# Performance work log

Measured on AMD Instinct MI355X. Metric: run time of the kernel, lower is better.

## Reference

```python
import jax, jax.numpy as jnp
import numpy as np

H = 128  # rnn_size

def _run_lstm(x, Wih, Whh, bih, bhh):
    # x: [B, T, D]; Wih: [4H, D]; Whh: [4H, H]; biases: [4H]
    B = x.shape[0]
    xg = jnp.einsum('btd,gd->btg', x, Wih) + bih + bhh  # precompute input projection [B,T,4H]
    WhhT = Whh.T  # [H, 4H]
    def step(carry, xg_t):
        h, c = carry
        g = xg_t + h @ WhhT  # [B, 4H]
        i = jax.nn.sigmoid(g[:, :H])
        f = jax.nn.sigmoid(g[:, H:2 * H])
        gg = jnp.tanh(g[:, 2 * H:3 * H])
        o = jax.nn.sigmoid(g[:, 3 * H:])
        c = f * c + i * gg
        h = o * jnp.tanh(c)
        return (h, c), h
    init = (jnp.zeros((B, H), x.dtype), jnp.zeros((B, H), x.dtype))
    _, ys = jax.lax.scan(step, init, jnp.swapaxes(xg, 0, 1))  # [T, B, H]
    return jnp.swapaxes(ys, 0, 1)  # [B, T, H]

def _bilstm(x, layers):
    h = x
    for (fw, bw) in layers:
        yf = _run_lstm(h, *fw)
        yb = jnp.flip(_run_lstm(jnp.flip(h, axis=1), *bw), axis=1)
        h = jnp.concatenate([yf, yb], axis=-1)  # [B, T, 2H]
    return h

def setup_inputs() -> dict:
    key = jax.random.key(0)
    ks = iter(jax.random.split(key, 32))
    B, T, D = 64, 512, 64
    s = 0.08  # init scale ~ 1/sqrt(H) to avoid gate saturation
    inp = {'x': jax.random.normal(next(ks), (B, T, D), jnp.float32)}
    for name, shape in [
        ('Wih00', (4 * H, D)), ('Whh00', (4 * H, H)), ('bih00', (4 * H,)), ('bhh00', (4 * H,)),
        ('Wih01', (4 * H, D)), ('Whh01', (4 * H, H)), ('bih01', (4 * H,)), ('bhh01', (4 * H,)),
        ('Wih10', (4 * H, 2 * H)), ('Whh10', (4 * H, H)), ('bih10', (4 * H,)), ('bhh10', (4 * H,)),
        ('Wih11', (4 * H, 2 * H)), ('Whh11', (4 * H, H)), ('bih11', (4 * H,)), ('bhh11', (4 * H,)),
        ('W1', (256, 2 * H)), ('b1', (256,)), ('W2', (D, 256)), ('b2', (D,)),
    ]:
        inp[name] = jax.random.normal(next(ks), shape, jnp.float32) * s
    return inp

def reference(x, Wih00, Whh00, bih00, bhh00, Wih01, Whh01, bih01, bhh01,
              Wih10, Whh10, bih10, bhh10, Wih11, Whh11, bih11, bhh11,
              W1, b1, W2, b2):
    layers = [((Wih00, Whh00, bih00, bhh00), (Wih01, Whh01, bih01, bhh01)),
              ((Wih10, Whh10, bih10, bhh10), (Wih11, Whh11, bih11, bhh11))]
    out = _bilstm(x, layers)  # [B, T, 2H]
    h = jax.nn.relu(jnp.einsum('bth,oh->bto', out, W1) + b1)
    return jnp.tanh(jnp.einsum('bth,oh->bto', h, W2) + b2)  # [B, T, input_size]
```

## Files before the change

### kernel.cpp

```cpp
#include <hip/hip_runtime.h>
#include <hip/hip_bf16.h>
#include <hip/hip_fp16.h>

typedef _Float16 h2vec __attribute__((ext_vector_type(2)));
typedef _Float16 f16x8 __attribute__((ext_vector_type(8)));
typedef float f32x4 __attribute__((ext_vector_type(4)));

static __device__ __forceinline__ float fast_sigmoid(float x) {
  return __builtin_amdgcn_rcpf(1.f + __expf(-x));
}
static __device__ __forceinline__ float fast_tanh(float x) {
  return 1.f - 2.f * __builtin_amdgcn_rcpf(__expf(2.f * x) + 1.f);
}
static __device__ __forceinline__ float fdot2u(unsigned int a, unsigned int b, float c) {
#if __has_builtin(__builtin_amdgcn_fdot2)
  return __builtin_amdgcn_fdot2(__builtin_bit_cast(h2vec, a),
                                __builtin_bit_cast(h2vec, b), c, false);
#else
  h2vec av = __builtin_bit_cast(h2vec, a);
  h2vec bv = __builtin_bit_cast(h2vec, b);
  return c + (float)av[0] * (float)bv[0] + (float)av[1] * (float)bv[1];
#endif
}
template<int CTRL>
static __device__ __forceinline__ float dpp_add(float v) {
  int x = __builtin_bit_cast(int, v);
  int y = __builtin_amdgcn_update_dpp(0, x, CTRL, 0xF, 0xF, true);
  return v + __builtin_bit_cast(float, y);
}
template<int CTRL>
static __device__ __forceinline__ float dpp_mov(float v) {
  int x = __builtin_bit_cast(int, v);
  int y = __builtin_amdgcn_update_dpp(0, x, CTRL, 0xF, 0xF, true);
  return __builtin_bit_cast(float, y);
}

template<int MODE>
__global__ __launch_bounds__(256) void gemm_mfma(
    const float* __restrict__ A, const float* __restrict__ W,
    const float* __restrict__ b0, const float* __restrict__ b1,
    float* __restrict__ C, int M, int N, int K) {
  __shared__ __align__(16) unsigned char As[128 * 128];
  __shared__ __align__(16) unsigned char Bs[64 * 128];
  const int tid = threadIdx.x;
  const int wave = tid >> 6, l = tid & 63;
  const int wm = wave >> 1, wn = wave & 1;
  const int m0 = blockIdx.x * 128, n0 = blockIdx.y * 64;
  const int lrow = l & 15, lq = l >> 4;

  f32x4 acc[4][2] = {};
  const int arow = tid >> 1, akc = (tid & 1) * 32;
  const int brow = tid >> 2, bkc = (tid & 3) * 16;

  for (int k0 = 0; k0 < K; k0 += 64) {
    {
      const float* src = A + (size_t)(m0 + arow) * K + k0 + akc;
#pragma unroll
      for (int u = 0; u < 4; ++u) {
        float4 v0 = *reinterpret_cast<const float4*>(src + u * 8);
        float4 v1 = *reinterpret_cast<const float4*>(src + u * 8 + 4);
        f16x8 h;
        h[0] = (_Float16)v0.x; h[1] = (_Float16)v0.y;
        h[2] = (_Float16)v0.z; h[3] = (_Float16)v0.w;
        h[4] = (_Float16)v1.x; h[5] = (_Float16)v1.y;
        h[6] = (_Float16)v1.z; h[7] = (_Float16)v1.w;
        const int kbyte = (akc + u * 8) * 2;
        *reinterpret_cast<f16x8*>(&As[arow * 128 + (kbyte ^ ((arow & 7) << 4))]) = h;
      }
    }
    {
      const float* src = W + (size_t)(n0 + brow) * K + k0 + bkc;
#pragma unroll
      for (int u = 0; u < 2; ++u) {
        float4 v0 = *reinterpret_cast<const float4*>(src + u * 8);
        float4 v1 = *reinterpret_cast<const float4*>(src + u * 8 + 4);
        f16x8 h;
        h[0] = (_Float16)v0.x; h[1] = (_Float16)v0.y;
        h[2] = (_Float16)v0.z; h[3] = (_Float16)v0.w;
        h[4] = (_Float16)v1.x; h[5] = (_Float16)v1.y;
        h[6] = (_Float16)v1.z; h[7] = (_Float16)v1.w;
        const int kbyte = (bkc + u * 8) * 2;
        *reinterpret_cast<f16x8*>(&Bs[brow * 128 + (kbyte ^ ((brow & 7) << 4))]) = h;
      }
    }
    __syncthreads();
#pragma unroll
    for (int kk = 0; kk < 64; kk += 32) {
      const int kbyte = (kk + lq * 8) * 2;
      f16x8 af[4], bf[2];
#pragma unroll
      for (int mt = 0; mt < 4; ++mt) {
        const int row = wm * 64 + mt * 16 + lrow;
        af[mt] = *reinterpret_cast<const f16x8*>(&As[row * 128 + (kbyte ^ ((row & 7) << 4))]);
      }
#pragma unroll
      for (int nt = 0; nt < 2; ++nt) {
        const int row = wn * 32 + nt * 16 + lrow;
        bf[nt] = *reinterpret_cast<const f16x8*>(&Bs[row * 128 + (kbyte ^ ((row & 7) << 4))]);
      }
#pragma unroll
      for (int mt = 0; mt < 4; ++mt)
#pragma unroll
        for (int nt = 0; nt < 2; ++nt)
          acc[mt][nt] = __builtin_amdgcn_mfma_f32_16x16x32_f16(af[mt], bf[nt], acc[mt][nt], 0, 0, 0);
    }
    __syncthreads();
  }

#pragma unroll
  for (int nt = 0; nt < 2; ++nt) {
    const int n = n0 + wn * 32 + nt * 16 + lrow;
    float bias = (MODE == 0) ? (b0[n] + b1[n]) : b0[n];
#pragma unroll
    for (int mt = 0; mt < 4; ++mt) {
#pragma unroll
      for (int r = 0; r < 4; ++r) {
        const int m = m0 + wm * 64 + mt * 16 + lq * 4 + r;
        float val = acc[mt][nt][r] + bias;
        if (MODE == 1) val = fmaxf(val, 0.f);
        if (MODE == 2) val = fast_tanh(val);
        C[(size_t)m * N + n] = val;
      }
    }
  }
}

__global__ __launch_bounds__(256) void gemm_proj_h(
    const float* __restrict__ A,
    const float* __restrict__ W0, const float* __restrict__ W1,
    const float* __restrict__ bi0, const float* __restrict__ bh0,
    const float* __restrict__ bi1, const float* __restrict__ bh1,
    __half* __restrict__ C0, __half* __restrict__ C1, int M, int N, int K) {
  const float* __restrict__ W  = blockIdx.z ? W1 : W0;
  const float* __restrict__ b0 = blockIdx.z ? bi1 : bi0;
  const float* __restrict__ b1 = blockIdx.z ? bh1 : bh0;
  __half* __restrict__ C = blockIdx.z ? C1 : C0;

  __shared__ __align__(16) unsigned char As[128 * 128];
  __shared__ __align__(16) unsigned char Bs[64 * 128];
  const int tid = threadIdx.x;
  const int wave = tid >> 6, l = tid & 63;
  const int wm = wave >> 1, wn = wave & 1;
  const int m0 = blockIdx.x * 128, n0 = blockIdx.y * 64;
  const int lrow = l & 15, lq = l >> 4;

  f32x4 acc[4][2] = {};
  const int arow = tid >> 1, akc = (tid & 1) * 32;
  const int brow = tid >> 2, bkc = (tid & 3) * 16;

  for (int k0 = 0; k0 < K; k0 += 64) {
    {
      const float* src = A + (size_t)(m0 + arow) * K + k0 + akc;
#pragma unroll
      for (int u = 0; u < 4; ++u) {
        float4 v0 = *reinterpret_cast<const float4*>(src + u * 8);
        float4 v1 = *reinterpret_cast<const float4*>(src + u * 8 + 4);
        f16x8 h;
        h[0] = (_Float16)v0.x; h[1] = (_Float16)v0.y;
        h[2] = (_Float16)v0.z; h[3] = (_Float16)v0.w;
        h[4] = (_Float16)v1.x; h[5] = (_Float16)v1.y;
        h[6] = (_Float16)v1.z; h[7] = (_Float16)v1.w;
        const int kbyte = (akc + u * 8) * 2;
        *reinterpret_cast<f16x8*>(&As[arow * 128 + (kbyte ^ ((arow & 7) << 4))]) = h;
      }
    }
    {
      const float* src = W + (size_t)(n0 + brow) * K + k0 + bkc;
#pragma unroll
      for (int u = 0; u < 2; ++u) {
        float4 v0 = *reinterpret_cast<const float4*>(src + u * 8);
        float4 v1 = *reinterpret_cast<const float4*>(src + u * 8 + 4);
        f16x8 h;
        h[0] = (_Float16)v0.x; h[1] = (_Float16)v0.y;
        h[2] = (_Float16)v0.z; h[3] = (_Float16)v0.w;
        h[4] = (_Float16)v1.x; h[5] = (_Float16)v1.y;
        h[6] = (_Float16)v1.z; h[7] = (_Float16)v1.w;
        const int kbyte = (bkc + u * 8) * 2;
        *reinterpret_cast<f16x8*>(&Bs[brow * 128 + (kbyte ^ ((brow & 7) << 4))]) = h;
      }
    }
    __syncthreads();
#pragma unroll
    for (int kk = 0; kk < 64; kk += 32) {
      const int kbyte = (kk + lq * 8) * 2;
      f16x8 af[4], bf[2];
#pragma unroll
      for (int mt = 0; mt < 4; ++mt) {
        const int row = wm * 64 + mt * 16 + lrow;
        af[mt] = *reinterpret_cast<const f16x8*>(&As[row * 128 + (kbyte ^ ((row & 7) << 4))]);
      }
#pragma unroll
      for (int nt = 0; nt < 2; ++nt) {
        const int row = wn * 32 + nt * 16 + lrow;
        bf[nt] = *reinterpret_cast<const f16x8*>(&Bs[row * 128 + (kbyte ^ ((row & 7) << 4))]);
      }
#pragma unroll
      for (int mt = 0; mt < 4; ++mt)
#pragma unroll
        for (int nt = 0; nt < 2; ++nt)
          acc[mt][nt] = __builtin_amdgcn_mfma_f32_16x16x32_f16(af[mt], bf[nt], acc[mt][nt], 0, 0, 0);
    }
    __syncthreads();
  }

#pragma unroll
  for (int nt = 0; nt < 2; ++nt) {
    const int n = n0 + wn * 32 + nt * 16 + lrow;
    const float bias = b0[n] + b1[n];
#pragma unroll
    for (int mt = 0; mt < 4; ++mt) {
#pragma unroll
      for (int r = 0; r < 4; ++r) {
        const int m = m0 + wm * 64 + mt * 16 + lq * 4 + r;
        C[(size_t)m * N + n] = __float2half_rn(acc[mt][nt][r] + bias);
      }
    }
  }
}

__global__ __launch_bounds__(512, 1) void lstm_seq6(
    const __half* __restrict__ xg_f, const __half* __restrict__ xg_b,
    const float* __restrict__ Whh_f, const float* __restrict__ Whh_b,
    float* __restrict__ out) {
  const int b = blockIdx.x;
  const int dir = blockIdx.y;
  const int tid = threadIdx.x;
  const int g6 = tid >> 3;
  const int e = tid & 7;
  const __half* __restrict__ xg = dir ? xg_b : xg_f;
  const float* __restrict__ Whh = dir ? Whh_b : Whh_f;

  __shared__ unsigned int hbuf[2][64];

  unsigned int w[4][2][8];
#pragma unroll
  for (int g = 0; g < 4; ++g)
#pragma unroll
    for (int u = 0; u < 2; ++u) {
      const float4* wr = reinterpret_cast<const float4*>(
          Whh + (size_t)(g * 128 + 2 * g6 + u) * 128 + e * 16);
#pragma unroll
      for (int q = 0; q < 4; ++q) {
        float4 v = wr[q];
        __half2 p0 = __floats2half2_rn(v.x, v.y);
        __half2 p1 = __floats2half2_rn(v.z, v.w);
        w[g][u][2 * q]     = __builtin_bit_cast(unsigned int, p0);
        w[g][u][2 * q + 1] = __builtin_bit_cast(unsigned int, p1);
      }
    }

  const int gate_e = (e < 4) ? (e >> 1) : (5 - (e >> 1));
  const int u_e = (e < 4) ? (e & 1) : ((e & 1) ^ 1);
  const int xidx = gate_e * 128 + 2 * g6 + u_e;

  if (tid < 128) reinterpret_cast<unsigned int*>(hbuf)[tid] = 0u;
  float c = 0.f;
  __syncthreads();

  const int tt0 = dir ? 511 : 0;
  const int stp = dir ? -1 : 1;
  const size_t base = (size_t)b * 512 * 512;

  unsigned short xva = __builtin_bit_cast(unsigned short, xg[base + (size_t)tt0 * 512 + xidx]);
  unsigned short xvb = __builtin_bit_cast(unsigned short, xg[base + (size_t)(tt0 + stp) * 512 + xidx]);

  auto step = [&](int t, unsigned int* rbuf, unsigned int* wbuf, unsigned short& xcur)
      __attribute__((always_inline)) {
    const int tt = tt0 + stp * t;

    const uint4* hc = reinterpret_cast<const uint4*>(&rbuf[e * 8]);
    uint4 q0 = hc[0], q1 = hc[1];
    unsigned int ha[8];
    ha[0] = q0.x; ha[1] = q0.y; ha[2] = q0.z; ha[3] = q0.w;
    ha[4] = q1.x; ha[5] = q1.y; ha[6] = q1.z; ha[7] = q1.w;

    float acc[4][2] = {};
#pragma unroll
    for (int kk = 0; kk < 8; ++kk) {
#pragma unroll
      for (int g = 0; g < 4; ++g) {
#pragma unroll
        for (int u = 0; u < 2; ++u)
          acc[g][u] = fdot2u(w[g][u][kk], ha[kk], acc[g][u]);
      }
    }

#pragma unroll
    for (int g = 0; g < 4; ++g)
#pragma unroll
      for (int u = 0; u < 2; ++u) {
        float a = acc[g][u];
        a = dpp_add<0xB1>(a);
        a = dpp_add<0x4E>(a);
        a = dpp_add<0x141>(a);
        acc[g][u] = a;
      }

    float a = acc[0][0];
    a = (e == 1) ? acc[0][1] : a;
    a = (e == 2) ? acc[1][0] : a;
    a = (e == 3) ? acc[1][1] : a;
    a = (e == 4) ? acc[3][1] : a;
    a = (e == 5) ? acc[3][0] : a;
    a = (e == 6) ? acc[2][1] : a;
    a = (e == 7) ? acc[2][0] : a;
    a += (float)__builtin_bit_cast(_Float16, xcur);

    {
      const int t2 = t + 2;
      const int tt2 = (t2 < 512) ? (tt0 + stp * t2) : tt0;
      xcur = __builtin_bit_cast(unsigned short, xg[base + (size_t)tt2 * 512 + xidx]);
    }

    const float xs = (e >= 6) ? 2.f * a : a;
    const float y = fast_sigmoid(xs);
    const float act = (e >= 6) ? 2.f * y - 1.f : y;

    const float m = dpp_mov<0x141>(act);
    const float fq = dpp_mov<0x4E>(act);
    const float oq = dpp_mov<0x4E>(m);

    c = fq * c + act * m;
    const float h = oq * (2.f * fast_sigmoid(2.f * c) - 1.f);

    if (e < 2) {
      unsigned short us = __builtin_bit_cast(unsigned short, (_Float16)h);
      reinterpret_cast<unsigned short*>(wbuf)[2 * g6 + e] = us;
      out[((size_t)b * 512 + tt) * 256 + dir * 128 + 2 * g6 + e] = h;
    }

    asm volatile("s_waitcnt lgkmcnt(0)" ::: "memory");
    __builtin_amdgcn_s_barrier();
    asm volatile("" ::: "memory");
  };

  for (int it = 0; it < 256; ++it) {
    step(2 * it,     hbuf[0], hbuf[1], xva);
    step(2 * it + 1, hbuf[1], hbuf[0], xvb);
  }
}

extern "C" void kernel_launch(void* const* d_in, const int* in_sizes, int n_in,
                              void* d_out, int out_size, void* d_ws, size_t ws_size,
                              hipStream_t stream) {
  (void)in_sizes; (void)n_in; (void)out_size; (void)ws_size;

  const float* x     = (const float*)d_in[0];
  const float* Wih00 = (const float*)d_in[1];
  const float* Whh00 = (const float*)d_in[2];
  const float* bih00 = (const float*)d_in[3];
  const float* bhh00 = (const float*)d_in[4];
  const float* Wih01 = (const float*)d_in[5];
  const float* Whh01 = (const float*)d_in[6];
  const float* bih01 = (const float*)d_in[7];
  const float* bhh01 = (const float*)d_in[8];
  const float* Wih10 = (const float*)d_in[9];
  const float* Whh10 = (const float*)d_in[10];
  const float* bih10 = (const float*)d_in[11];
  const float* bhh10 = (const float*)d_in[12];
  const float* Wih11 = (const float*)d_in[13];
  const float* Whh11 = (const float*)d_in[14];
  const float* bih11 = (const float*)d_in[15];
  const float* bhh11 = (const float*)d_in[16];
  const float* W1 = (const float*)d_in[17];
  const float* b1 = (const float*)d_in[18];
  const float* W2 = (const float*)d_in[19];
  const float* b2 = (const float*)d_in[20];
  float* out = (float*)d_out;

  char* ws = (char*)d_ws;
  __half* xgh_f = (__half*)ws;
  __half* xgh_b = (__half*)(ws + ((size_t)32 << 20));
  float*  buf   = (float*)(ws + ((size_t)64 << 20));
  float*  tmp   = (float*)(ws + ((size_t)96 << 20));

  const int M = 64 * 512;

  gemm_proj_h<<<dim3(M / 128, 8, 2), 256, 0, stream>>>(
      x, Wih00, Wih01, bih00, bhh00, bih01, bhh01, xgh_f, xgh_b, M, 512, 64);
  lstm_seq6<<<dim3(64, 2), 512, 0, stream>>>(xgh_f, xgh_b, Whh00, Whh01, buf);

  gemm_proj_h<<<dim3(M / 128, 8, 2), 256, 0, stream>>>(
      buf, Wih10, Wih11, bih10, bhh10, bih11, bhh11, xgh_f, xgh_b, M, 512, 256);
  lstm_seq6<<<dim3(64, 2), 512, 0, stream>>>(xgh_f, xgh_b, Whh10, Whh11, buf);

  gemm_mfma<1><<<dim3(M / 128, 4), 256, 0, stream>>>(
      buf, W1, b1, nullptr, tmp, M, 256, 256);
  gemm_mfma<2><<<dim3(M / 128, 1), 256, 0, stream>>>(
      tmp, W2, b2, nullptr, out, M, 64, 256);
}
```

Measured before the change: 760.8 us.

## Batch 16 sequences per block and compute LSTM recurrence with MFMA

The recurrent LSTM kernel is rewritten so that each block handles 16 batch sequences instead of one. The h·Whh^T product is computed with 16x16x32 f16 MFMA instructions, replacing the per-thread fdot2 plus DPP reduction. Each lane now evaluates all four gates for four hidden units, so the cross-lane shuffles before the cell update go away. Hidden state is exchanged through a swizzled LDS buffer, and loads of the input projection and stores of the output are vectorised. The grid shrinks from 128 blocks to 8, so only a few compute units do the serial work, and per-step latency now depends on chains of dependent MFMAs and on more transcendental work per lane.

```diff
diff --git a/kernel.cpp b/kernel.cpp
--- a/kernel.cpp
+++ b/kernel.cpp
@@ -3,6 +3,7 @@
 #include <hip/hip_fp16.h>
 
 typedef _Float16 h2vec __attribute__((ext_vector_type(2)));
+typedef _Float16 f16x4 __attribute__((ext_vector_type(4)));
 typedef _Float16 f16x8 __attribute__((ext_vector_type(8)));
 typedef float f32x4 __attribute__((ext_vector_type(4)));
 
@@ -11,28 +12,6 @@
 }
 static __device__ __forceinline__ float fast_tanh(float x) {
   return 1.f - 2.f * __builtin_amdgcn_rcpf(__expf(2.f * x) + 1.f);
-}
-static __device__ __forceinline__ float fdot2u(unsigned int a, unsigned int b, float c) {
-#if __has_builtin(__builtin_amdgcn_fdot2)
-  return __builtin_amdgcn_fdot2(__builtin_bit_cast(h2vec, a),
-                                __builtin_bit_cast(h2vec, b), c, false);
-#else
-  h2vec av = __builtin_bit_cast(h2vec, a);
-  h2vec bv = __builtin_bit_cast(h2vec, b);
-  return c + (float)av[0] * (float)bv[0] + (float)av[1] * (float)bv[1];
-#endif
-}
-template<int CTRL>
-static __device__ __forceinline__ float dpp_add(float v) {
-  int x = __builtin_bit_cast(int, v);
-  int y = __builtin_amdgcn_update_dpp(0, x, CTRL, 0xF, 0xF, true);
-  return v + __builtin_bit_cast(float, y);
-}
-template<int CTRL>
-static __device__ __forceinline__ float dpp_mov(float v) {
-  int x = __builtin_bit_cast(int, v);
-  int y = __builtin_amdgcn_update_dpp(0, x, CTRL, 0xF, 0xF, true);
-  return __builtin_bit_cast(float, y);
 }
 
 template<int MODE>
@@ -218,116 +197,108 @@
   }
 }
 
-__global__ __launch_bounds__(512, 1) void lstm_seq6(
+__global__ __launch_bounds__(512, 1) void lstm_mfma2(
     const __half* __restrict__ xg_f, const __half* __restrict__ xg_b,
     const float* __restrict__ Whh_f, const float* __restrict__ Whh_b,
     float* __restrict__ out) {
-  const int b = blockIdx.x;
+  const int bt = blockIdx.x;
   const int dir = blockIdx.y;
   const int tid = threadIdx.x;
-  const int g6 = tid >> 3;
-  const int e = tid & 7;
+  const int w = tid >> 6;
+  const int l = tid & 63;
+  const int col = l & 15;
+  const int q = l >> 4;
+
   const __half* __restrict__ xg = dir ? xg_b : xg_f;
   const float* __restrict__ Whh = dir ? Whh_b : Whh_f;
 
-  __shared__ unsigned int hbuf[2][64];
-
-  unsigned int w[4][2][8];
-#pragma unroll
-  for (int g = 0; g < 4; ++g)
-#pragma unroll
-    for (int u = 0; u < 2; ++u) {
-      const float4* wr = reinterpret_cast<const float4*>(
-          Whh + (size_t)(g * 128 + 2 * g6 + u) * 128 + e * 16);
-#pragma unroll
-      for (int q = 0; q < 4; ++q) {
-        float4 v = wr[q];
-        __half2 p0 = __floats2half2_rn(v.x, v.y);
-        __half2 p1 = __floats2half2_rn(v.z, v.w);
-        w[g][u][2 * q]     = __builtin_bit_cast(unsigned int, p0);
-        w[g][u][2 * q + 1] = __builtin_bit_cast(unsigned int, p1);
-      }
-    }
-
-  const int gate_e = (e < 4) ? (e >> 1) : (5 - (e >> 1));
-  const int u_e = (e < 4) ? (e & 1) : ((e & 1) ^ 1);
-  const int xidx = gate_e * 128 + 2 * g6 + u_e;
-
-  if (tid < 128) reinterpret_cast<unsigned int*>(hbuf)[tid] = 0u;
-  float c = 0.f;
+  __shared__ __align__(16) unsigned char h_lds[2][16 * 256];
+
+  f16x8 a[4][4];
+#pragma unroll
+  for (int g = 0; g < 4; ++g) {
+    const int gate = (g * 8 + w) * 16 + col;
+#pragma unroll
+    for (int kf = 0; kf < 4; ++kf) {
+      const float* p = Whh + (size_t)gate * 128 + kf * 32 + q * 8;
+      float4 v0 = *reinterpret_cast<const float4*>(p);
+      float4 v1 = *reinterpret_cast<const float4*>(p + 4);
+      f16x8 av;
+      av[0] = (_Float16)v0.x; av[1] = (_Float16)v0.y;
+      av[2] = (_Float16)v0.z; av[3] = (_Float16)v0.w;
+      av[4] = (_Float16)v1.x; av[5] = (_Float16)v1.y;
+      av[6] = (_Float16)v1.z; av[7] = (_Float16)v1.w;
+      a[g][kf] = av;
+    }
+  }
+
+  for (int i = tid; i < (int)(sizeof(h_lds) / 4); i += 512)
+    reinterpret_cast<unsigned int*>(h_lds)[i] = 0u;
+  f32x4 c4 = {0.f, 0.f, 0.f, 0.f};
   __syncthreads();
 
   const int tt0 = dir ? 511 : 0;
   const int stp = dir ? -1 : 1;
-  const size_t base = (size_t)b * 512 * 512;
-
-  unsigned short xva = __builtin_bit_cast(unsigned short, xg[base + (size_t)tt0 * 512 + xidx]);
-  unsigned short xvb = __builtin_bit_cast(unsigned short, xg[base + (size_t)(tt0 + stp) * 512 + xidx]);
-
-  auto step = [&](int t, unsigned int* rbuf, unsigned int* wbuf, unsigned short& xcur)
+  const int b_glob = bt * 16 + col;
+  const size_t xbase = (size_t)b_glob * 512 * 512;
+  const int goff = w * 16 + q * 4;
+  const int swz = (col & 7) << 4;
+
+  struct XReg { f16x4 v[4]; };
+  XReg xva, xvb;
+#pragma unroll
+  for (int g = 0; g < 4; ++g) {
+    xva.v[g] = *reinterpret_cast<const f16x4*>(xg + xbase + (size_t)tt0 * 512 + g * 128 + goff);
+    xvb.v[g] = *reinterpret_cast<const f16x4*>(xg + xbase + (size_t)(tt0 + stp) * 512 + g * 128 + goff);
+  }
+
+  auto step = [&](int t, unsigned char* rbuf, unsigned char* wbuf, XReg& xcur)
       __attribute__((always_inline)) {
     const int tt = tt0 + stp * t;
 
-    const uint4* hc = reinterpret_cast<const uint4*>(&rbuf[e * 8]);
-    uint4 q0 = hc[0], q1 = hc[1];
-    unsigned int ha[8];
-    ha[0] = q0.x; ha[1] = q0.y; ha[2] = q0.z; ha[3] = q0.w;
-    ha[4] = q1.x; ha[5] = q1.y; ha[6] = q1.z; ha[7] = q1.w;
-
-    float acc[4][2] = {};
-#pragma unroll
-    for (int kk = 0; kk < 8; ++kk) {
-#pragma unroll
-      for (int g = 0; g < 4; ++g) {
-#pragma unroll
-        for (int u = 0; u < 2; ++u)
-          acc[g][u] = fdot2u(w[g][u][kk], ha[kk], acc[g][u]);
-      }
-    }
-
-#pragma unroll
-    for (int g = 0; g < 4; ++g)
-#pragma unroll
-      for (int u = 0; u < 2; ++u) {
-        float a = acc[g][u];
-        a = dpp_add<0xB1>(a);
-        a = dpp_add<0x4E>(a);
-        a = dpp_add<0x141>(a);
-        acc[g][u] = a;
-      }
-
-    float a = acc[0][0];
-    a = (e == 1) ? acc[0][1] : a;
-    a = (e == 2) ? acc[1][0] : a;
-    a = (e == 3) ? acc[1][1] : a;
-    a = (e == 4) ? acc[3][1] : a;
-    a = (e == 5) ? acc[3][0] : a;
-    a = (e == 6) ? acc[2][1] : a;
-    a = (e == 7) ? acc[2][0] : a;
-    a += (float)__builtin_bit_cast(_Float16, xcur);
+    f16x8 bf[4];
+#pragma unroll
+    for (int kf = 0; kf < 4; ++kf) {
+      const int byte = ((kf * 32 + q * 8) * 2) ^ swz;
+      bf[kf] = *reinterpret_cast<const f16x8*>(&rbuf[col * 256 + byte]);
+    }
+
+    f32x4 acc[4] = {{0.f,0.f,0.f,0.f},{0.f,0.f,0.f,0.f},
+                    {0.f,0.f,0.f,0.f},{0.f,0.f,0.f,0.f}};
+#pragma unroll
+    for (int kf = 0; kf < 4; ++kf) {
+#pragma unroll
+      for (int g = 0; g < 4; ++g)
+        acc[g] = __builtin_amdgcn_mfma_f32_16x16x32_f16(a[g][kf], bf[kf], acc[g], 0, 0, 0);
+    }
+
+    f16x4 hpack;
+    float hout[4];
+#pragma unroll
+    for (int r = 0; r < 4; ++r) {
+      const float gi = fast_sigmoid(acc[0][r] + (float)xcur.v[0][r]);
+      const float gf = fast_sigmoid(acc[1][r] + (float)xcur.v[1][r]);
+      const float gg = fast_tanh(acc[2][r] + (float)xcur.v[2][r]);
+      const float go = fast_sigmoid(acc[3][r] + (float)xcur.v[3][r]);
+      c4[r] = gf * c4[r] + gi * gg;
+      const float h = go * fast_tanh(c4[r]);
+      hpack[r] = (_Float16)h;
+      hout[r] = h;
+    }
 
     {
       const int t2 = t + 2;
       const int tt2 = (t2 < 512) ? (tt0 + stp * t2) : tt0;
-      xcur = __builtin_bit_cast(unsigned short, xg[base + (size_t)tt2 * 512 + xidx]);
-    }
-
-    const float xs = (e >= 6) ? 2.f * a : a;
-    const float y = fast_sigmoid(xs);
-    const float act = (e >= 6) ? 2.f * y - 1.f : y;
-
-    const float m = dpp_mov<0x141>(act);
-    const float fq = dpp_mov<0x4E>(act);
-    const float oq = dpp_mov<0x4E>(m);
-
-    c = fq * c + act * m;
-    const float h = oq * (2.f * fast_sigmoid(2.f * c) - 1.f);
-
-    if (e < 2) {
-      unsigned short us = __builtin_bit_cast(unsigned short, (_Float16)h);
-      reinterpret_cast<unsigned short*>(wbuf)[2 * g6 + e] = us;
-      out[((size_t)b * 512 + tt) * 256 + dir * 128 + 2 * g6 + e] = h;
-    }
+#pragma unroll
+      for (int g = 0; g < 4; ++g)
+        xcur.v[g] = *reinterpret_cast<const f16x4*>(
+            xg + xbase + (size_t)tt2 * 512 + g * 128 + goff);
+    }
+
+    *reinterpret_cast<f16x4*>(&wbuf[col * 256 + ((goff * 2) ^ swz)]) = hpack;
+
+    *reinterpret_cast<float4*>(out + ((size_t)b_glob * 512 + tt) * 256 + dir * 128 + goff)
+        = make_float4(hout[0], hout[1], hout[2], hout[3]);
 
     asm volatile("s_waitcnt lgkmcnt(0)" ::: "memory");
     __builtin_amdgcn_s_barrier();
@@ -335,8 +306,8 @@
   };
 
   for (int it = 0; it < 256; ++it) {
-    step(2 * it,     hbuf[0], hbuf[1], xva);
-    step(2 * it + 1, hbuf[1], hbuf[0], xvb);
+    step(2 * it,     h_lds[0], h_lds[1], xva);
+    step(2 * it + 1, h_lds[1], h_lds[0], xvb);
   }
 }
 
@@ -378,11 +349,11 @@
 
   gemm_proj_h<<<dim3(M / 128, 8, 2), 256, 0, stream>>>(
       x, Wih00, Wih01, bih00, bhh00, bih01, bhh01, xgh_f, xgh_b, M, 512, 64);
-  lstm_seq6<<<dim3(64, 2), 512, 0, stream>>>(xgh_f, xgh_b, Whh00, Whh01, buf);
+  lstm_mfma2<<<dim3(4, 2), 512, 0, stream>>>(xgh_f, xgh_b, Whh00, Whh01, buf);
 
   gemm_proj_h<<<dim3(M / 128, 8, 2), 256, 0, stream>>>(
       buf, Wih10, Wih11, bih10, bhh10, bih11, bhh11, xgh_f, xgh_b, M, 512, 256);
-  lstm_seq6<<<dim3(64, 2), 512, 0, stream>>>(xgh_f, xgh_b, Whh10, Whh11, buf);
+  lstm_mfma2<<<dim3(4, 2), 512, 0, stream>>>(xgh_f, xgh_b, Whh10, Whh11, buf);
 
   gemm_mfma<1><<<dim3(M / 128, 4), 256, 0, stream>>>(
       buf, W1, b1, nullptr, tmp, M, 256, 256);
```

New measurement: 1.129 ms. +48.3%, slower.

## Remap LSTM threads to one unit per quad and store intermediates as fp16

Applied to the files above, without the earlier changes.

The recurrent kernel now gives each hidden unit four lanes. Each lane covers a 32-wide k slice for all four gates, so the cross-lane reduction needs two DPP steps instead of three. Gate values are then gathered with quad-broadcast DPP. Intermediate activations between stages (the LSTM outputs and the MLP hidden layer) are stored as fp16, which halves global traffic, and the GEMMs read fp16 inputs directly. Launch bounds now allow two blocks per CU, and the output store is moved to a different lane than the LDS write. This adds fp16 rounding on intermediates, although the GEMMs already converted their inputs to fp16.

```diff
diff --git a/kernel.cpp b/kernel.cpp
--- a/kernel.cpp
+++ b/kernel.cpp
@@ -35,11 +35,33 @@
   return __builtin_bit_cast(float, y);
 }
 
-template<int MODE>
-__global__ __launch_bounds__(256) void gemm_mfma(
-    const float* __restrict__ A, const float* __restrict__ W,
+template<typename AT>
+static __device__ __forceinline__ void stage_row32(
+    const AT* __restrict__ src, unsigned char* __restrict__ dst,
+    int row, int kc ) {
+#pragma unroll
+  for (int u = 0; u < 4; ++u) {
+    f16x8 h;
+    if constexpr (sizeof(AT) == 4) {
+      float4 v0 = *reinterpret_cast<const float4*>((const float*)src + u * 8);
+      float4 v1 = *reinterpret_cast<const float4*>((const float*)src + u * 8 + 4);
+      h[0] = (_Float16)v0.x; h[1] = (_Float16)v0.y;
+      h[2] = (_Float16)v0.z; h[3] = (_Float16)v0.w;
+      h[4] = (_Float16)v1.x; h[5] = (_Float16)v1.y;
+      h[6] = (_Float16)v1.z; h[7] = (_Float16)v1.w;
+    } else {
+      h = *reinterpret_cast<const f16x8*>((const __half*)src + u * 8);
+    }
+    const int kbyte = (kc + u * 8) * 2;
+    *reinterpret_cast<f16x8*>(&dst[row * 128 + (kbyte ^ ((row & 7) << 4))]) = h;
+  }
+}
+
+template<typename AT, typename OT, int MODE>
+__global__ __launch_bounds__(256) void gemm_mfma2(
+    const AT* __restrict__ A, const float* __restrict__ W,
     const float* __restrict__ b0, const float* __restrict__ b1,
-    float* __restrict__ C, int M, int N, int K) {
+    OT* __restrict__ C, int M, int N, int K) {
   __shared__ __align__(16) unsigned char As[128 * 128];
   __shared__ __align__(16) unsigned char Bs[64 * 128];
   const int tid = threadIdx.x;
@@ -53,21 +75,7 @@
   const int brow = tid >> 2, bkc = (tid & 3) * 16;
 
   for (int k0 = 0; k0 < K; k0 += 64) {
-    {
-      const float* src = A + (size_t)(m0 + arow) * K + k0 + akc;
-#pragma unroll
-      for (int u = 0; u < 4; ++u) {
-        float4 v0 = *reinterpret_cast<const float4*>(src + u * 8);
-        float4 v1 = *reinterpret_cast<const float4*>(src + u * 8 + 4);
-        f16x8 h;
-        h[0] = (_Float16)v0.x; h[1] = (_Float16)v0.y;
-        h[2] = (_Float16)v0.z; h[3] = (_Float16)v0.w;
-        h[4] = (_Float16)v1.x; h[5] = (_Float16)v1.y;
-        h[6] = (_Float16)v1.z; h[7] = (_Float16)v1.w;
-        const int kbyte = (akc + u * 8) * 2;
-        *reinterpret_cast<f16x8*>(&As[arow * 128 + (kbyte ^ ((arow & 7) << 4))]) = h;
-      }
-    }
+    stage_row32<AT>(A + (size_t)(m0 + arow) * K + k0 + akc, As, arow, akc);
     {
       const float* src = W + (size_t)(n0 + brow) * K + k0 + bkc;
 #pragma unroll
@@ -119,14 +127,18 @@
         float val = acc[mt][nt][r] + bias;
         if (MODE == 1) val = fmaxf(val, 0.f);
         if (MODE == 2) val = fast_tanh(val);
-        C[(size_t)m * N + n] = val;
-      }
-    }
-  }
-}
-
+        if constexpr (sizeof(OT) == 2)
+          C[(size_t)m * N + n] = __float2half_rn(val);
+        else
+          C[(size_t)m * N + n] = val;
+      }
+    }
+  }
+}
+
+template<typename AT>
 __global__ __launch_bounds__(256) void gemm_proj_h(
-    const float* __restrict__ A,
+    const AT* __restrict__ A,
     const float* __restrict__ W0, const float* __restrict__ W1,
     const float* __restrict__ bi0, const float* __restrict__ bh0,
     const float* __restrict__ bi1, const float* __restrict__ bh1,
@@ -149,21 +161,7 @@
   const int brow = tid >> 2, bkc = (tid & 3) * 16;
 
   for (int k0 = 0; k0 < K; k0 += 64) {
-    {
-      const float* src = A + (size_t)(m0 + arow) * K + k0 + akc;
-#pragma unroll
-      for (int u = 0; u < 4; ++u) {
-        float4 v0 = *reinterpret_cast<const float4*>(src + u * 8);
-        float4 v1 = *reinterpret_cast<const float4*>(src + u * 8 + 4);
-        f16x8 h;
-        h[0] = (_Float16)v0.x; h[1] = (_Float16)v0.y;
-        h[2] = (_Float16)v0.z; h[3] = (_Float16)v0.w;
-        h[4] = (_Float16)v1.x; h[5] = (_Float16)v1.y;
-        h[6] = (_Float16)v1.z; h[7] = (_Float16)v1.w;
-        const int kbyte = (akc + u * 8) * 2;
-        *reinterpret_cast<f16x8*>(&As[arow * 128 + (kbyte ^ ((arow & 7) << 4))]) = h;
-      }
-    }
+    stage_row32<AT>(A + (size_t)(m0 + arow) * K + k0 + akc, As, arow, akc);
     {
       const float* src = W + (size_t)(n0 + brow) * K + k0 + bkc;
 #pragma unroll
@@ -218,48 +216,43 @@
   }
 }
 
-__global__ __launch_bounds__(512, 1) void lstm_seq6(
+__global__ __launch_bounds__(512, 2) void lstm_seq5h(
     const __half* __restrict__ xg_f, const __half* __restrict__ xg_b,
     const float* __restrict__ Whh_f, const float* __restrict__ Whh_b,
-    float* __restrict__ out) {
+    __half* __restrict__ out) {
   const int b = blockIdx.x;
   const int dir = blockIdx.y;
   const int tid = threadIdx.x;
-  const int g6 = tid >> 3;
-  const int e = tid & 7;
+  const int j = tid >> 2;
+  const int kq = tid & 3;
   const __half* __restrict__ xg = dir ? xg_b : xg_f;
   const float* __restrict__ Whh = dir ? Whh_b : Whh_f;
 
   __shared__ unsigned int hbuf[2][64];
 
-  unsigned int w[4][2][8];
-#pragma unroll
-  for (int g = 0; g < 4; ++g)
-#pragma unroll
-    for (int u = 0; u < 2; ++u) {
-      const float4* wr = reinterpret_cast<const float4*>(
-          Whh + (size_t)(g * 128 + 2 * g6 + u) * 128 + e * 16);
-#pragma unroll
-      for (int q = 0; q < 4; ++q) {
-        float4 v = wr[q];
-        __half2 p0 = __floats2half2_rn(v.x, v.y);
-        __half2 p1 = __floats2half2_rn(v.z, v.w);
-        w[g][u][2 * q]     = __builtin_bit_cast(unsigned int, p0);
-        w[g][u][2 * q + 1] = __builtin_bit_cast(unsigned int, p1);
-      }
-    }
-
-  const int gate_e = (e < 4) ? (e >> 1) : (5 - (e >> 1));
-  const int u_e = (e < 4) ? (e & 1) : ((e & 1) ^ 1);
-  const int xidx = gate_e * 128 + 2 * g6 + u_e;
-
-  if (tid < 128) reinterpret_cast<unsigned int*>(hbuf)[tid] = 0u;
+  unsigned int w[4][16];
+#pragma unroll
+  for (int g = 0; g < 4; ++g) {
+    const float4* wr = reinterpret_cast<const float4*>(
+        Whh + (size_t)(g * 128 + j) * 128 + kq * 32);
+#pragma unroll
+    for (int q = 0; q < 8; ++q) {
+      float4 v = wr[q];
+      __half2 p0 = __floats2half2_rn(v.x, v.y);
+      __half2 p1 = __floats2half2_rn(v.z, v.w);
+      w[g][2 * q]     = __builtin_bit_cast(unsigned int, p0);
+      w[g][2 * q + 1] = __builtin_bit_cast(unsigned int, p1);
+    }
+  }
+
+  if (tid < 128) hbuf[tid >> 6][tid & 63] = 0u;
   float c = 0.f;
   __syncthreads();
 
   const int tt0 = dir ? 511 : 0;
   const int stp = dir ? -1 : 1;
   const size_t base = (size_t)b * 512 * 512;
+  const int xidx = kq * 128 + j;
 
   unsigned short xva = __builtin_bit_cast(unsigned short, xg[base + (size_t)tt0 * 512 + xidx]);
   unsigned short xvb = __builtin_bit_cast(unsigned short, xg[base + (size_t)(tt0 + stp) * 512 + xidx]);
@@ -268,42 +261,34 @@
       __attribute__((always_inline)) {
     const int tt = tt0 + stp * t;
 
-    const uint4* hc = reinterpret_cast<const uint4*>(&rbuf[e * 8]);
-    uint4 q0 = hc[0], q1 = hc[1];
-    unsigned int ha[8];
+    const uint4* hc = reinterpret_cast<const uint4*>(&rbuf[kq * 16]);
+    uint4 q0 = hc[0], q1 = hc[1], q2 = hc[2], q3 = hc[3];
+    unsigned int ha[16];
     ha[0] = q0.x; ha[1] = q0.y; ha[2] = q0.z; ha[3] = q0.w;
     ha[4] = q1.x; ha[5] = q1.y; ha[6] = q1.z; ha[7] = q1.w;
-
-    float acc[4][2] = {};
-#pragma unroll
-    for (int kk = 0; kk < 8; ++kk) {
-#pragma unroll
-      for (int g = 0; g < 4; ++g) {
-#pragma unroll
-        for (int u = 0; u < 2; ++u)
-          acc[g][u] = fdot2u(w[g][u][kk], ha[kk], acc[g][u]);
-      }
-    }
-
-#pragma unroll
-    for (int g = 0; g < 4; ++g)
-#pragma unroll
-      for (int u = 0; u < 2; ++u) {
-        float a = acc[g][u];
-        a = dpp_add<0xB1>(a);
-        a = dpp_add<0x4E>(a);
-        a = dpp_add<0x141>(a);
-        acc[g][u] = a;
-      }
-
-    float a = acc[0][0];
-    a = (e == 1) ? acc[0][1] : a;
-    a = (e == 2) ? acc[1][0] : a;
-    a = (e == 3) ? acc[1][1] : a;
-    a = (e == 4) ? acc[3][1] : a;
-    a = (e == 5) ? acc[3][0] : a;
-    a = (e == 6) ? acc[2][1] : a;
-    a = (e == 7) ? acc[2][0] : a;
+    ha[8] = q2.x; ha[9] = q2.y; ha[10] = q2.z; ha[11] = q2.w;
+    ha[12] = q3.x; ha[13] = q3.y; ha[14] = q3.z; ha[15] = q3.w;
+
+    float acc[4] = {0.f, 0.f, 0.f, 0.f};
+#pragma unroll
+    for (int kk = 0; kk < 16; ++kk) {
+#pragma unroll
+      for (int g = 0; g < 4; ++g)
+        acc[g] = fdot2u(w[g][kk], ha[kk], acc[g]);
+    }
+
+#pragma unroll
+    for (int g = 0; g < 4; ++g) {
+      float a = acc[g];
+      a = dpp_add<0xB1>(a);
+      a = dpp_add<0x4E>(a);
+      acc[g] = a;
+    }
+
+    float a = acc[0];
+    a = (kq == 1) ? acc[1] : a;
+    a = (kq == 2) ? acc[2] : a;
+    a = (kq == 3) ? acc[3] : a;
     a += (float)__builtin_bit_cast(_Float16, xcur);
 
     {
@@ -312,21 +297,24 @@
       xcur = __builtin_bit_cast(unsigned short, xg[base + (size_t)tt2 * 512 + xidx]);
     }
 
-    const float xs = (e >= 6) ? 2.f * a : a;
+    const float xs = (kq == 2) ? 2.f * a : a;
     const float y = fast_sigmoid(xs);
-    const float act = (e >= 6) ? 2.f * y - 1.f : y;
-
-    const float m = dpp_mov<0x141>(act);
-    const float fq = dpp_mov<0x4E>(act);
-    const float oq = dpp_mov<0x4E>(m);
-
-    c = fq * c + act * m;
-    const float h = oq * (2.f * fast_sigmoid(2.f * c) - 1.f);
-
-    if (e < 2) {
+    const float act = (kq == 2) ? 2.f * y - 1.f : y;
+
+    const float gi = dpp_mov<0x00>(act);
+    const float gf = dpp_mov<0x55>(act);
+    const float gg = dpp_mov<0xAA>(act);
+    const float go = dpp_mov<0xFF>(act);
+
+    c = gf * c + gi * gg;
+    const float h = go * (2.f * fast_sigmoid(2.f * c) - 1.f);
+
+    if (kq == 0) {
       unsigned short us = __builtin_bit_cast(unsigned short, (_Float16)h);
-      reinterpret_cast<unsigned short*>(wbuf)[2 * g6 + e] = us;
-      out[((size_t)b * 512 + tt) * 256 + dir * 128 + 2 * g6 + e] = h;
+      reinterpret_cast<unsigned short*>(wbuf)[j] = us;
+    }
+    if (kq == 1) {
+      out[((size_t)b * 512 + tt) * 256 + dir * 128 + j] = __float2half_rn(h);
     }
 
     asm volatile("s_waitcnt lgkmcnt(0)" ::: "memory");
@@ -371,21 +359,21 @@
   char* ws = (char*)d_ws;
   __half* xgh_f = (__half*)ws;
   __half* xgh_b = (__half*)(ws + ((size_t)32 << 20));
-  float*  buf   = (float*)(ws + ((size_t)64 << 20));
-  float*  tmp   = (float*)(ws + ((size_t)96 << 20));
+  __half* bufh  = (__half*)(ws + ((size_t)64 << 20));
+  __half* tmph  = (__half*)(ws + ((size_t)80 << 20));
 
   const int M = 64 * 512;
 
-  gemm_proj_h<<<dim3(M / 128, 8, 2), 256, 0, stream>>>(
+  gemm_proj_h<float><<<dim3(M / 128, 8, 2), 256, 0, stream>>>(
       x, Wih00, Wih01, bih00, bhh00, bih01, bhh01, xgh_f, xgh_b, M, 512, 64);
-  lstm_seq6<<<dim3(64, 2), 512, 0, stream>>>(xgh_f, xgh_b, Whh00, Whh01, buf);
-
-  gemm_proj_h<<<dim3(M / 128, 8, 2), 256, 0, stream>>>(
-      buf, Wih10, Wih11, bih10, bhh10, bih11, bhh11, xgh_f, xgh_b, M, 512, 256);
-  lstm_seq6<<<dim3(64, 2), 512, 0, stream>>>(xgh_f, xgh_b, Whh10, Whh11, buf);
-
-  gemm_mfma<1><<<dim3(M / 128, 4), 256, 0, stream>>>(
-      buf, W1, b1, nullptr, tmp, M, 256, 256);
-  gemm_mfma<2><<<dim3(M / 128, 1), 256, 0, stream>>>(
-      tmp, W2, b2, nullptr, out, M, 64, 256);
-}
+  lstm_seq5h<<<dim3(64, 2), 512, 0, stream>>>(xgh_f, xgh_b, Whh00, Whh01, bufh);
+
+  gemm_proj_h<__half><<<dim3(M / 128, 8, 2), 256, 0, stream>>>(
+      bufh, Wih10, Wih11, bih10, bhh10, bih11, bhh11, xgh_f, xgh_b, M, 512, 256);
+  lstm_seq5h<<<dim3(64, 2), 512, 0, stream>>>(xgh_f, xgh_b, Whh10, Whh11, bufh);
+
+  gemm_mfma2<__half, __half, 1><<<dim3(M / 128, 4), 256, 0, stream>>>(
+      bufh, W1, b1, nullptr, tmph, M, 256, 256);
+  gemm_mfma2<__half, float, 2><<<dim3(M / 128, 1), 256, 0, stream>>>(
+      tmph, W2, b2, nullptr, out, M, 64, 256);
+}
```

After: 629.9 us. 1.21x faster.
